# Kernel tuning notes

Measured on AMD Instinct MI355X. Metric: run time of the kernel, lower is better.

Reference implementation:

```python
import jax, jax.numpy as jnp
import numpy as np

B, HW, C = 128, 1024, 384

def setup_inputs() -> dict:
    key = jax.random.key(0)
    k1, k2, k3 = jax.random.split(key, 3)
    x = jax.random.normal(k1, (B, HW + 1, C), dtype=jnp.float32)
    cls_token = jax.random.normal(k2, (B, 1, C), dtype=jnp.float32)
    edge_aggregation = jax.random.normal(k3, (B, HW, C), dtype=jnp.float32)
    return {"x": x, "cls_token": cls_token, "edge_aggregation": edge_aggregation, "pool": 1}


def reference(x, cls_token, edge_aggregation, pool):
    # edge_aggregation: (B, HW, C) -> avgpool over HW -> (B, 1, C)
    ea = jnp.mean(edge_aggregation, axis=1, keepdims=True)
    channel_importance = jax.nn.sigmoid(ea)                      # (B, 1, C)
    nodes = x[:, 1:]                                             # (B, HW, C)
    # channel_aggregation: nodes @ channel_importance^T -> (B, HW, 1)
    channel_aggregation = jnp.einsum('bnc,bc->bn', nodes, channel_importance[:, 0])[..., None]
    node_importance = jax.nn.sigmoid(channel_aggregation)        # (B, HW, 1)
    # node_aggregation: node_importance^T @ nodes -> (B, 1, C)
    node_aggregation = jnp.einsum('bn,bnc->bc', node_importance[..., 0], nodes)[:, None, :]
    # global (Frobenius) 2-norms, matching torch .norm(2) over the whole tensor
    normalization = jnp.linalg.norm(cls_token) / jnp.linalg.norm(node_aggregation)
    cls_token_out = cls_token + normalization * node_aggregation  # (B, 1, C)
    if pool:
        # ascending sort by channel_aggregation, keep top quarter (largest importance)
        idx = jnp.argsort(channel_aggregation[..., 0], axis=1)    # (B, HW)
        nodes_sorted = jnp.take_along_axis(nodes, idx[..., None], axis=1)
        hw = nodes.shape[1]
        nodes_pooled = nodes_sorted[:, hw // 4 * 3:]              # (B, HW/4, C)
        out = jnp.concatenate([cls_token_out, nodes_pooled], axis=1)
    else:
        out = jnp.concatenate([cls_token_out, nodes], axis=1)
    return out
```

## Files before the change

kernel.cpp:

```cpp
#include <hip/hip_runtime.h>
#include <math.h>

#define B 128
#define N 1024
#define C 384
#define C4 96
#define NS 8
#define RPT (N / NS)
#define XROWS 1025
#define OUTROWS 257

typedef float f32x4 __attribute__((ext_vector_type(4)));

#define OFF_EAP  0
#define SZ_EAP   (B * NS * C)
#define OFF_NA   (OFF_EAP + SZ_EAP)
#define SZ_NA    (B * C)
#define OFF_SQ   (OFF_NA + SZ_NA)
#define SZ_SQ    (2 * B)

__device__ __forceinline__ float sigmoidf(float v) { return 1.f / (1.f + expf(-v)); }
__device__ __forceinline__ float dot4v(f32x4 a, f32x4 b) {
    return a.x * b.x + a.y * b.y + a.z * b.z + a.w * b.w;
}

__global__ __launch_bounds__(384) void k1_ea_partial(const float* __restrict__ ea,
                                                     float* __restrict__ eaP) {
    int b = blockIdx.x, s = blockIdx.y, t = threadIdx.x;
    int rg = t / C4, c4 = t % C4;
    const f32x4* p = (const f32x4*)(ea + ((size_t)b * N + (size_t)s * RPT) * C);
    f32x4 acc = (f32x4)(0.f);
#pragma unroll 8
    for (int it = 0; it < RPT / 4; ++it)
        acc += __builtin_nontemporal_load(&p[(size_t)(it * 4 + rg) * C4 + c4]);
    __shared__ f32x4 lds[4][C4];
    lds[rg][c4] = acc;
    __syncthreads();
    if (t < C4) {
        f32x4 r = lds[0][t] + lds[1][t] + lds[2][t] + lds[3][t];
        ((f32x4*)(eaP + ((size_t)b * NS + s) * C))[t] = r;
    }
}

__global__ __launch_bounds__(1024) void fatk(const float* __restrict__ x,
                                             const float* __restrict__ cls,
                                             const float* __restrict__ eaP,
                                             float* __restrict__ na,
                                             float* __restrict__ sqp,
                                             float* __restrict__ out) {
    int b = blockIdx.x, tid = threadIdx.x;
    int w = tid >> 6, lane = tid & 63, hl = lane & 31, half = lane >> 5;

    __shared__ f32x4 eap[NS][C4];
    __shared__ float sci[C];
    __shared__ float dots[N];
    __shared__ f32x4 sacc[16][C4];
    __shared__ unsigned long long bufA[N];
    __shared__ unsigned long long bufB[N];
    __shared__ unsigned llist[256];

    if (tid < NS * C4) {
        int rg = tid / C4, c4 = tid % C4;
        eap[rg][c4] = ((const f32x4*)(eaP + ((size_t)b * NS + rg) * C))[c4];
    }
    __syncthreads();
    if (tid < C4) {
        f32x4 s = (f32x4)(0.f);
#pragma unroll
        for (int r = 0; r < NS; ++r) s += eap[r][tid];
        s *= (1.f / (float)N);
        sci[4 * tid + 0] = sigmoidf(s.x);
        sci[4 * tid + 1] = sigmoidf(s.y);
        sci[4 * tid + 2] = sigmoidf(s.z);
        sci[4 * tid + 3] = sigmoidf(s.w);
    }
    __syncthreads();

    f32x4 cir[3];
#pragma unroll
    for (int k = 0; k < 3; ++k) cir[k] = ((const f32x4*)sci)[hl + 32 * k];
    f32x4 acc[3];
#pragma unroll
    for (int k = 0; k < 3; ++k) acc[k] = (f32x4)(0.f);

    const float* xb = x + (size_t)b * XROWS * C + C;
#pragma unroll 2
    for (int it = 0; it < 32; ++it) {
        int r = 32 * it + 2 * w + half;
        const f32x4* rp = (const f32x4*)(xb + (size_t)r * C);
        f32x4 v[3];
        float dotv = 0.f;
#pragma unroll
        for (int k = 0; k < 3; ++k) {
            v[k] = rp[hl + 32 * k];
            dotv += dot4v(v[k], cir[k]);
        }
#pragma unroll
        for (int off = 16; off > 0; off >>= 1) dotv += __shfl_xor(dotv, off, 64);
        if (hl == 0) dots[r] = dotv;
        float si = sigmoidf(dotv);
#pragma unroll
        for (int k = 0; k < 3; ++k) acc[k] += si * v[k];
    }
#pragma unroll
    for (int k = 0; k < 3; ++k) {
        acc[k].x += __shfl_xor(acc[k].x, 32, 64);
        acc[k].y += __shfl_xor(acc[k].y, 32, 64);
        acc[k].z += __shfl_xor(acc[k].z, 32, 64);
        acc[k].w += __shfl_xor(acc[k].w, 32, 64);
    }
    if (half == 0) {
#pragma unroll
        for (int k = 0; k < 3; ++k) sacc[w][hl + 32 * k] = acc[k];
    }
    __syncthreads();

    float* escr = (float*)&eap[0][0];
    if (tid < C4) {
        f32x4 s = (f32x4)(0.f);
#pragma unroll
        for (int w2 = 0; w2 < 16; ++w2) s += sacc[w2][tid];
        ((f32x4*)(na + (size_t)b * C))[tid] = s;
        escr[tid] = dot4v(s, s);
        f32x4 cv = ((const f32x4*)(cls + (size_t)b * C))[tid];
        escr[C4 + tid] = dot4v(cv, cv);
    }
    __syncthreads();
    if (w == 0) {
        float nss = (lane < 32) ? (escr[lane] + escr[lane + 32] + escr[lane + 64]) : 0.f;
        float css = (lane < 32) ? (escr[C4 + lane] + escr[C4 + lane + 32] + escr[C4 + lane + 64]) : 0.f;
#pragma unroll
        for (int off = 32; off > 0; off >>= 1) {
            nss += __shfl_xor(nss, off, 64);
            css += __shfl_xor(css, off, 64);
        }
        if (lane == 0) { sqp[b] = nss; sqp[B + b] = css; }
    }

    float vv = dots[tid];
    unsigned u = __float_as_uint(vv);
    u = (u & 0x80000000u) ? ~u : (u | 0x80000000u);
    unsigned long long key = ((unsigned long long)u << 32) | (unsigned)tid;

    bool useA = true;
    for (int k = 2; k <= N; k <<= 1) {
        bool up = ((tid & k) == 0);
        for (int j = k >> 1; j > 0; j >>= 1) {
            unsigned long long other;
            if (j < 64) {
                other = __shfl_xor(key, j, 64);
            } else {
                unsigned long long* buf = useA ? bufA : bufB;
                useA = !useA;
                buf[tid] = key;
                __syncthreads();
                other = buf[tid ^ j];
            }
            bool iAmLow = ((tid & j) == 0);
            bool keepMin = (iAmLow == up);
            bool otherLess = (other < key);
            key = (keepMin == otherLess) ? other : key;
        }
    }
    __syncthreads();

    unsigned* flag = (unsigned*)bufA;
    unsigned* wsum = (unsigned*)bufB;
    flag[tid] = 0;
    __syncthreads();
    if (tid >= 768) flag[(unsigned)(key & 1023u)] = (unsigned)(tid - 768) | 0x80000000u;
    __syncthreads();
    unsigned f = flag[tid];
    bool sel = (f & 0x80000000u) != 0;
    unsigned long long bal = __ballot(sel);
    if (lane == 0) wsum[w] = (unsigned)__popcll(bal);
    __syncthreads();
    if (sel) {
        int base = 0;
        for (int w2 = 0; w2 < w; ++w2) base += (int)wsum[w2];
        int intra = (int)__popcll(bal & ((1ull << lane) - 1ull));
        llist[base + intra] = ((unsigned)tid << 8) | (f & 0xFFu);
    }
    __syncthreads();

    const float* xb2 = x + ((size_t)b * XROWS + 1) * C;
#pragma unroll 4
    for (int q = 0; q < 24; ++q) {
        int e = tid + 1024 * q;
        int lp = e / C4, c4 = e % C4;
        unsigned ent = llist[lp];
        int node = (int)(ent >> 8);
        int op = (int)(ent & 0xFFu);
        f32x4 sv = *((const f32x4*)(xb2 + (size_t)node * C) + c4);
        __builtin_nontemporal_store(sv,
            (f32x4*)(out + ((size_t)b * OUTROWS + 1 + op) * C) + c4);
    }
}

__global__ __launch_bounds__(384) void kZ_cls(const float* __restrict__ sqp,
                                              const float* __restrict__ cls,
                                              const float* __restrict__ na,
                                              float* __restrict__ out) {
    int b = blockIdx.x, t = threadIdx.x;
    __shared__ float2 red[128];
    if (t < 128) red[t] = make_float2(sqp[t], sqp[B + t]);
    __syncthreads();
    for (int o = 64; o > 0; o >>= 1) {
        if (t < o) {
            float2 a = red[t], d = red[t + o];
            red[t] = make_float2(a.x + d.x, a.y + d.y);
        }
        __syncthreads();
    }
    float ratio = sqrtf(red[0].y / red[0].x);
    out[((size_t)b * OUTROWS) * C + t] =
        cls[(size_t)b * C + t] + ratio * na[(size_t)b * C + t];
}

extern "C" void kernel_launch(void* const* d_in, const int* in_sizes, int n_in,
                              void* d_out, int out_size, void* d_ws, size_t ws_size,
                              hipStream_t stream) {
    const float* x   = (const float*)d_in[0];
    const float* cls = (const float*)d_in[1];
    const float* ea  = (const float*)d_in[2];
    float* out = (float*)d_out;
    float* ws  = (float*)d_ws;

    float* eaP = ws + OFF_EAP;
    float* na  = ws + OFF_NA;
    float* sqp = ws + OFF_SQ;

    k1_ea_partial<<<dim3(B, NS), 384, 0, stream>>>(ea, eaP);
    fatk<<<B, 1024, 0, stream>>>(x, cls, eaP, na, sqp, out);
    kZ_cls<<<B, 384, 0, stream>>>(sqp, cls, na, out);
}
```

Baseline: 90.41 us.

## Split fused per-batch kernel into x-pass and sort/gather kernels with more blocks

```diff
diff --git a/kernel.cpp b/kernel.cpp
--- a/kernel.cpp
+++ b/kernel.cpp
@@ -14,17 +14,21 @@
 
 #define OFF_EAP  0
 #define SZ_EAP   (B * NS * C)
-#define OFF_NA   (OFF_EAP + SZ_EAP)
+#define OFF_NAP  (OFF_EAP + SZ_EAP)
+#define SZ_NAP   (B * 2 * C)
+#define OFF_NA   (OFF_NAP + SZ_NAP)
 #define SZ_NA    (B * C)
 #define OFF_SQ   (OFF_NA + SZ_NA)
 #define SZ_SQ    (2 * B)
+#define OFF_DOTS (OFF_SQ + SZ_SQ)
+#define SZ_DOTS  (B * N)
 
 __device__ __forceinline__ float sigmoidf(float v) { return 1.f / (1.f + expf(-v)); }
 __device__ __forceinline__ float dot4v(f32x4 a, f32x4 b) {
     return a.x * b.x + a.y * b.y + a.z * b.z + a.w * b.w;
 }
 
-__global__ __launch_bounds__(384) void k1_ea_partial(const float* __restrict__ ea,
+__global__ __launch_bounds__(384) void kA_ea_partial(const float* __restrict__ ea,
                                                      float* __restrict__ eaP) {
     int b = blockIdx.x, s = blockIdx.y, t = threadIdx.x;
     int rg = t / C4, c4 = t % C4;
@@ -42,32 +46,21 @@
     }
 }
 
-__global__ __launch_bounds__(1024) void fatk(const float* __restrict__ x,
-                                             const float* __restrict__ cls,
-                                             const float* __restrict__ eaP,
-                                             float* __restrict__ na,
-                                             float* __restrict__ sqp,
-                                             float* __restrict__ out) {
-    int b = blockIdx.x, tid = threadIdx.x;
+__global__ __launch_bounds__(1024) void kB_xpass(const float* __restrict__ x,
+                                                 const float* __restrict__ eaP,
+                                                 float* __restrict__ naP,
+                                                 float* __restrict__ dotsG) {
+    int b = blockIdx.x, sb = blockIdx.y, tid = threadIdx.x;
     int w = tid >> 6, lane = tid & 63, hl = lane & 31, half = lane >> 5;
 
-    __shared__ f32x4 eap[NS][C4];
     __shared__ float sci[C];
-    __shared__ float dots[N];
     __shared__ f32x4 sacc[16][C4];
-    __shared__ unsigned long long bufA[N];
-    __shared__ unsigned long long bufB[N];
-    __shared__ unsigned llist[256];
-
-    if (tid < NS * C4) {
-        int rg = tid / C4, c4 = tid % C4;
-        eap[rg][c4] = ((const f32x4*)(eaP + ((size_t)b * NS + rg) * C))[c4];
-    }
-    __syncthreads();
+
     if (tid < C4) {
+        const f32x4* ep = (const f32x4*)(eaP + (size_t)b * NS * C);
         f32x4 s = (f32x4)(0.f);
 #pragma unroll
-        for (int r = 0; r < NS; ++r) s += eap[r][tid];
+        for (int r = 0; r < NS; ++r) s += ep[(size_t)r * C4 + tid];
         s *= (1.f / (float)N);
         sci[4 * tid + 0] = sigmoidf(s.x);
         sci[4 * tid + 1] = sigmoidf(s.y);
@@ -83,9 +76,9 @@
 #pragma unroll
     for (int k = 0; k < 3; ++k) acc[k] = (f32x4)(0.f);
 
-    const float* xb = x + (size_t)b * XROWS * C + C;
+    const float* xb = x + (size_t)b * XROWS * C + C + (size_t)sb * 512 * C;
 #pragma unroll 2
-    for (int it = 0; it < 32; ++it) {
+    for (int it = 0; it < 16; ++it) {
         int r = 32 * it + 2 * w + half;
         const f32x4* rp = (const f32x4*)(xb + (size_t)r * C);
         f32x4 v[3];
@@ -97,7 +90,7 @@
         }
 #pragma unroll
         for (int off = 16; off > 0; off >>= 1) dotv += __shfl_xor(dotv, off, 64);
-        if (hl == 0) dots[r] = dotv;
+        if (hl == 0) dotsG[(size_t)b * N + sb * 512 + r] = dotv;
         float si = sigmoidf(dotv);
 #pragma unroll
         for (int k = 0; k < 3; ++k) acc[k] += si * v[k];
@@ -115,29 +108,53 @@
     }
     __syncthreads();
 
-    float* escr = (float*)&eap[0][0];
     if (tid < C4) {
         f32x4 s = (f32x4)(0.f);
 #pragma unroll
         for (int w2 = 0; w2 < 16; ++w2) s += sacc[w2][tid];
-        ((f32x4*)(na + (size_t)b * C))[tid] = s;
-        escr[tid] = dot4v(s, s);
-        f32x4 cv = ((const f32x4*)(cls + (size_t)b * C))[tid];
-        escr[C4 + tid] = dot4v(cv, cv);
-    }
-    __syncthreads();
-    if (w == 0) {
-        float nss = (lane < 32) ? (escr[lane] + escr[lane + 32] + escr[lane + 64]) : 0.f;
-        float css = (lane < 32) ? (escr[C4 + lane] + escr[C4 + lane + 32] + escr[C4 + lane + 64]) : 0.f;
-#pragma unroll
-        for (int off = 32; off > 0; off >>= 1) {
-            nss += __shfl_xor(nss, off, 64);
-            css += __shfl_xor(css, off, 64);
-        }
-        if (lane == 0) { sqp[b] = nss; sqp[B + b] = css; }
-    }
-
-    float vv = dots[tid];
+        ((f32x4*)(naP + ((size_t)b * 2 + sb) * C))[tid] = s;
+    }
+}
+
+__global__ __launch_bounds__(1024) void kC_sort_gather(const float* __restrict__ x,
+                                                       const float* __restrict__ cls,
+                                                       const float* __restrict__ naP,
+                                                       const float* __restrict__ dotsG,
+                                                       float* __restrict__ na,
+                                                       float* __restrict__ sqp,
+                                                       float* __restrict__ out) {
+    int b = blockIdx.x, g = blockIdx.y, tid = threadIdx.x;
+    int w = tid >> 6, lane = tid & 63;
+
+    __shared__ unsigned long long bufA[N];
+    __shared__ unsigned long long bufB[N];
+    __shared__ unsigned llist[256];
+    __shared__ float escr[2 * C4];
+
+    if (g == 0) {
+        if (tid < C4) {
+            const f32x4* p0 = (const f32x4*)(naP + (size_t)b * 2 * C);
+            const f32x4* p1 = (const f32x4*)(naP + ((size_t)b * 2 + 1) * C);
+            f32x4 s = p0[tid] + p1[tid];
+            ((f32x4*)(na + (size_t)b * C))[tid] = s;
+            escr[tid] = dot4v(s, s);
+            f32x4 cv = ((const f32x4*)(cls + (size_t)b * C))[tid];
+            escr[C4 + tid] = dot4v(cv, cv);
+        }
+        __syncthreads();
+        if (w == 0) {
+            float nss = (lane < 32) ? (escr[lane] + escr[lane + 32] + escr[lane + 64]) : 0.f;
+            float css = (lane < 32) ? (escr[C4 + lane] + escr[C4 + lane + 32] + escr[C4 + lane + 64]) : 0.f;
+#pragma unroll
+            for (int off = 32; off > 0; off >>= 1) {
+                nss += __shfl_xor(nss, off, 64);
+                css += __shfl_xor(css, off, 64);
+            }
+            if (lane == 0) { sqp[b] = nss; sqp[B + b] = css; }
+        }
+    }
+
+    float vv = dotsG[(size_t)b * N + tid];
     unsigned u = __float_as_uint(vv);
     u = (u & 0x80000000u) ? ~u : (u | 0x80000000u);
     unsigned long long key = ((unsigned long long)u << 32) | (unsigned)tid;
@@ -185,9 +202,9 @@
 
     const float* xb2 = x + ((size_t)b * XROWS + 1) * C;
 #pragma unroll 4
-    for (int q = 0; q < 24; ++q) {
+    for (int q = 0; q < 12; ++q) {
         int e = tid + 1024 * q;
-        int lp = e / C4, c4 = e % C4;
+        int lp = 128 * g + e / C4, c4 = e % C4;
         unsigned ent = llist[lp];
         int node = (int)(ent >> 8);
         int op = (int)(ent & 0xFFu);
@@ -226,11 +243,14 @@
     float* out = (float*)d_out;
     float* ws  = (float*)d_ws;
 
-    float* eaP = ws + OFF_EAP;
-    float* na  = ws + OFF_NA;
-    float* sqp = ws + OFF_SQ;
-
-    k1_ea_partial<<<dim3(B, NS), 384, 0, stream>>>(ea, eaP);
-    fatk<<<B, 1024, 0, stream>>>(x, cls, eaP, na, sqp, out);
+    float* eaP   = ws + OFF_EAP;
+    float* naP   = ws + OFF_NAP;
+    float* na    = ws + OFF_NA;
+    float* sqp   = ws + OFF_SQ;
+    float* dotsG = ws + OFF_DOTS;
+
+    kA_ea_partial<<<dim3(B, NS), 384, 0, stream>>>(ea, eaP);
+    kB_xpass<<<dim3(B, 2), 1024, 0, stream>>>(x, eaP, naP, dotsG);
+    kC_sort_gather<<<dim3(B, 2), 1024, 0, stream>>>(x, cls, naP, dotsG, na, sqp, out);
     kZ_cls<<<B, 384, 0, stream>>>(sqp, cls, na, out);
 }
```

Result: slower. 95.31 us (+5.4%).

## Fuse edge-aggregation mean reduction into main per-batch kernel

Applied to the files above, without the earlier changes.

```diff
diff --git a/kernel.cpp b/kernel.cpp
--- a/kernel.cpp
+++ b/kernel.cpp
@@ -5,16 +5,12 @@
 #define N 1024
 #define C 384
 #define C4 96
-#define NS 8
-#define RPT (N / NS)
 #define XROWS 1025
 #define OUTROWS 257
 
 typedef float f32x4 __attribute__((ext_vector_type(4)));
 
-#define OFF_EAP  0
-#define SZ_EAP   (B * NS * C)
-#define OFF_NA   (OFF_EAP + SZ_EAP)
+#define OFF_NA   0
 #define SZ_NA    (B * C)
 #define OFF_SQ   (OFF_NA + SZ_NA)
 #define SZ_SQ    (2 * B)
@@ -24,50 +20,53 @@
     return a.x * b.x + a.y * b.y + a.z * b.z + a.w * b.w;
 }
 
-__global__ __launch_bounds__(384) void k1_ea_partial(const float* __restrict__ ea,
-                                                     float* __restrict__ eaP) {
-    int b = blockIdx.x, s = blockIdx.y, t = threadIdx.x;
-    int rg = t / C4, c4 = t % C4;
-    const f32x4* p = (const f32x4*)(ea + ((size_t)b * N + (size_t)s * RPT) * C);
-    f32x4 acc = (f32x4)(0.f);
-#pragma unroll 8
-    for (int it = 0; it < RPT / 4; ++it)
-        acc += __builtin_nontemporal_load(&p[(size_t)(it * 4 + rg) * C4 + c4]);
-    __shared__ f32x4 lds[4][C4];
-    lds[rg][c4] = acc;
-    __syncthreads();
-    if (t < C4) {
-        f32x4 r = lds[0][t] + lds[1][t] + lds[2][t] + lds[3][t];
-        ((f32x4*)(eaP + ((size_t)b * NS + s) * C))[t] = r;
-    }
-}
-
 __global__ __launch_bounds__(1024) void fatk(const float* __restrict__ x,
                                              const float* __restrict__ cls,
-                                             const float* __restrict__ eaP,
+                                             const float* __restrict__ ea,
                                              float* __restrict__ na,
                                              float* __restrict__ sqp,
                                              float* __restrict__ out) {
     int b = blockIdx.x, tid = threadIdx.x;
     int w = tid >> 6, lane = tid & 63, hl = lane & 31, half = lane >> 5;
 
-    __shared__ f32x4 eap[NS][C4];
     __shared__ float sci[C];
     __shared__ float dots[N];
     __shared__ f32x4 sacc[16][C4];
     __shared__ unsigned long long bufA[N];
     __shared__ unsigned long long bufB[N];
     __shared__ unsigned llist[256];
-
-    if (tid < NS * C4) {
-        int rg = tid / C4, c4 = tid % C4;
-        eap[rg][c4] = ((const f32x4*)(eaP + ((size_t)b * NS + rg) * C))[c4];
+    __shared__ float escr[2 * C4];
+
+    {
+        const float* eb = ea + (size_t)b * N * C;
+        f32x4 eacc[3];
+#pragma unroll
+        for (int k = 0; k < 3; ++k) eacc[k] = (f32x4)(0.f);
+#pragma unroll 2
+        for (int it = 0; it < 32; ++it) {
+            int r = 32 * it + 2 * w + half;
+            const f32x4* rp = (const f32x4*)(eb + (size_t)r * C);
+#pragma unroll
+            for (int k = 0; k < 3; ++k)
+                eacc[k] += __builtin_nontemporal_load(&rp[hl + 32 * k]);
+        }
+#pragma unroll
+        for (int k = 0; k < 3; ++k) {
+            eacc[k].x += __shfl_xor(eacc[k].x, 32, 64);
+            eacc[k].y += __shfl_xor(eacc[k].y, 32, 64);
+            eacc[k].z += __shfl_xor(eacc[k].z, 32, 64);
+            eacc[k].w += __shfl_xor(eacc[k].w, 32, 64);
+        }
+        if (half == 0) {
+#pragma unroll
+            for (int k = 0; k < 3; ++k) sacc[w][hl + 32 * k] = eacc[k];
+        }
     }
     __syncthreads();
     if (tid < C4) {
         f32x4 s = (f32x4)(0.f);
 #pragma unroll
-        for (int r = 0; r < NS; ++r) s += eap[r][tid];
+        for (int w2 = 0; w2 < 16; ++w2) s += sacc[w2][tid];
         s *= (1.f / (float)N);
         sci[4 * tid + 0] = sigmoidf(s.x);
         sci[4 * tid + 1] = sigmoidf(s.y);
@@ -115,7 +114,6 @@
     }
     __syncthreads();
 
-    float* escr = (float*)&eap[0][0];
     if (tid < C4) {
         f32x4 s = (f32x4)(0.f);
 #pragma unroll
@@ -226,11 +224,9 @@
     float* out = (float*)d_out;
     float* ws  = (float*)d_ws;
 
-    float* eaP = ws + OFF_EAP;
     float* na  = ws + OFF_NA;
     float* sqp = ws + OFF_SQ;
 
-    k1_ea_partial<<<dim3(B, NS), 384, 0, stream>>>(ea, eaP);
-    fatk<<<B, 1024, 0, stream>>>(x, cls, eaP, na, sqp, out);
+    fatk<<<B, 1024, 0, stream>>>(x, cls, ea, na, sqp, out);
     kZ_cls<<<B, 384, 0, stream>>>(sqp, cls, na, out);
 }
```

Result: slower. 92.69 us (+2.5%).
